# Optimization experiments

Measured on AMD Instinct MI355X. Metric: run time of the kernel, lower is better.

The kernel has to match this reference:

```python
import jax, jax.numpy as jnp
import numpy as np

N, D = 8192, 2        # n_samples, embedding dim (== init dim)
K = 32                # k_base with strategy='fixed' -> static topk size
ALPHA = 1.0           # alpha.item() in forward -> constant
NOISE_SCALE = 0.01
EPS = 1e-8


def setup_inputs() -> dict:
    key = jax.random.key(0)
    x = jax.random.normal(key, (N, D), dtype=jnp.float32)
    return {"x": x}


def _forward(x):
    # torch.std is unbiased (ddof=1)
    mean = jnp.mean(x, axis=0, keepdims=True)          # [1, D]
    std = jnp.std(x, axis=0, keepdims=True, ddof=1)    # [1, D]
    xc = x - mean

    # pairwise Euclidean distances (torch.cdist, p=2): [N, N]
    sq = jnp.sum(xc * xc, axis=1)
    d2 = sq[:, None] + sq[None, :] - 2.0 * (xc @ xc.T)
    dists = jnp.sqrt(jnp.maximum(d2, 0.0))

    # kth-smallest distance per row -> per-point bandwidth sigma
    neg_topk, _ = jax.lax.top_k(-dists, K)             # smallest K (incl. self)
    sigma = -neg_topk[:, -1][:, None]                  # [N, 1]

    # adaptive-bandwidth kernel, row-normalized
    kernel = jnp.exp(-dists / (2.0 * sigma ** 2 + EPS))
    kernel = kernel / (jnp.sum(kernel, axis=1, keepdims=True) + EPS)

    drift = kernel @ xc                                # [N, D]

    step = float(D) ** (-ALPHA)                        # dim ** (-alpha)
    noise = jax.random.normal(jax.random.key(42), xc.shape, dtype=xc.dtype) * NOISE_SCALE
    h = xc + step * (drift - xc) + noise

    # restore original per-feature scale and location
    cur_std = jnp.std(h, axis=0, keepdims=True, ddof=1)
    h = h * (std / (cur_std + EPS))
    return h + mean


def reference(x):
    return _forward(x)
```

## Files before the change

kernel.cpp:

```cpp
#include <hip/hip_runtime.h>
#include <stdint.h>
#include <math.h>

#define N_PTS 8192
#define WPB   16
#define TPB   (WPB * 64)
#define NBLK  (N_PTS / WPB)
#define GRIDC 64
#define NCELL (GRIDC * GRIDC)
#define CW    (9.0f / 64.0f)
#define CINV  (64.0f / 9.0f)

typedef __fp16 h2 __attribute__((ext_vector_type(2)));
typedef uint32_t u32;

__device__ __forceinline__ u32 pksub(u32 a, u32 b) {
  u32 d;
  asm("v_pk_add_f16 %0, %1, %2 neg_lo:[0,1] neg_hi:[0,1]" : "=v"(d) : "v"(a), "v"(b));
  return d;
}
__device__ __forceinline__ float dot2u(u32 a, u32 b, float c) {
#if __has_builtin(__builtin_amdgcn_fdot2)
  return __builtin_amdgcn_fdot2(__builtin_bit_cast(h2, a), __builtin_bit_cast(h2, b), c, false);
#else
  h2 x = __builtin_bit_cast(h2, a), y = __builtin_bit_cast(h2, b);
  return fmaf((float)x.x, (float)y.x, fmaf((float)x.y, (float)y.y, c));
#endif
}
__device__ __forceinline__ u32 cvtpk(float a, float b) {
  return __builtin_bit_cast(u32, __builtin_amdgcn_cvt_pkrtz(a, b));
}
__device__ __forceinline__ int cellc(float v) {
  int c = (int)floorf((v + 4.5f) * CINV);
  return c < 0 ? 0 : (c > GRIDC - 1 ? GRIDC - 1 : c);
}

__device__ __forceinline__ uint32_t rotl32(uint32_t x, int r) {
  return (x << r) | (x >> (32 - r));
}
__device__ __forceinline__ uint32_t threefry_bits(uint32_t idx) {
  const uint32_t k0 = 0u, k1 = 42u;
  const uint32_t k2c = k0 ^ k1 ^ 0x1BD11BDAu;
  uint32_t x0 = 0u, x1 = idx;
  x0 += k0; x1 += k1;
  x0 += x1; x1 = rotl32(x1, 13); x1 ^= x0;
  x0 += x1; x1 = rotl32(x1, 15); x1 ^= x0;
  x0 += x1; x1 = rotl32(x1, 26); x1 ^= x0;
  x0 += x1; x1 = rotl32(x1,  6); x1 ^= x0;
  x0 += k1; x1 += k2c + 1u;
  x0 += x1; x1 = rotl32(x1, 17); x1 ^= x0;
  x0 += x1; x1 = rotl32(x1, 29); x1 ^= x0;
  x0 += x1; x1 = rotl32(x1, 16); x1 ^= x0;
  x0 += x1; x1 = rotl32(x1, 24); x1 ^= x0;
  x0 += k2c; x1 += k0 + 2u;
  x0 += x1; x1 = rotl32(x1, 13); x1 ^= x0;
  x0 += x1; x1 = rotl32(x1, 15); x1 ^= x0;
  x0 += x1; x1 = rotl32(x1, 26); x1 ^= x0;
  x0 += x1; x1 = rotl32(x1,  6); x1 ^= x0;
  x0 += k0; x1 += k1 + 3u;
  x0 += x1; x1 = rotl32(x1, 17); x1 ^= x0;
  x0 += x1; x1 = rotl32(x1, 29); x1 ^= x0;
  x0 += x1; x1 = rotl32(x1, 16); x1 ^= x0;
  x0 += x1; x1 = rotl32(x1, 24); x1 ^= x0;
  x0 += k1; x1 += k2c + 4u;
  x0 += x1; x1 = rotl32(x1, 13); x1 ^= x0;
  x0 += x1; x1 = rotl32(x1, 15); x1 ^= x0;
  x0 += x1; x1 = rotl32(x1, 26); x1 ^= x0;
  x0 += x1; x1 = rotl32(x1,  6); x1 ^= x0;
  x0 += k2c; x1 += k0 + 5u;
  return x0 ^ x1;
}
__device__ __forceinline__ float erfinv_xla(float x) {
  float w = -log1pf(-x * x);
  float p;
  if (w < 5.0f) {
    w -= 2.5f;
    p = 2.81022636e-08f;
    p = fmaf(p, w, 3.43273939e-07f);
    p = fmaf(p, w, -3.5233877e-06f);
    p = fmaf(p, w, -4.39150654e-06f);
    p = fmaf(p, w, 0.00021858087f);
    p = fmaf(p, w, -0.00125372503f);
    p = fmaf(p, w, -0.00417768164f);
    p = fmaf(p, w, 0.246640727f);
    p = fmaf(p, w, 1.50140941f);
  } else {
    w = sqrtf(w) - 3.0f;
    p = -0.000200214257f;
    p = fmaf(p, w, 0.000100950558f);
    p = fmaf(p, w, 0.00134934322f);
    p = fmaf(p, w, -0.00367342844f);
    p = fmaf(p, w, 0.00573950773f);
    p = fmaf(p, w, -0.0076224613f);
    p = fmaf(p, w, 0.00943887047f);
    p = fmaf(p, w, 1.00167406f);
    p = fmaf(p, w, 2.83297682f);
  }
  return p * x;
}
__device__ __forceinline__ float jax_noise(uint32_t idx) {
  uint32_t bits = threefry_bits(idx);
  float uf = __uint_as_float((bits >> 9) | 0x3F800000u) - 1.0f;
  const float lo_u = -0.99999994f;
  float u = fmaxf(lo_u, fmaf(uf, 2.0f, lo_u));
  return 1.4142135623730951f * erfinv_xla(u) * 0.01f;
}

__global__ __launch_bounds__(1024) void build1_kernel(const float* __restrict__ x,
                                                      float* __restrict__ stats,
                                                      u32* __restrict__ base,
                                                      u32* __restrict__ cursor,
                                                      u32* __restrict__ iimg) {
  __shared__ u32 baseL[NCELL];
  __shared__ u32 ssc[1024];
  __shared__ double sred[16][4];
  const int t = threadIdx.x;

#pragma unroll
  for (int k = 0; k < 4; ++k) baseL[t * 4 + k] = 0;
  __syncthreads();

  double s0 = 0, s1 = 0, q0 = 0, q1 = 0;
#pragma unroll
  for (int k = 0; k < 8; ++k) {
    float2 p = ((const float2*)x)[t * 8 + k];
    int cell = cellc(p.y) * GRIDC + cellc(p.x);
    atomicAdd(&baseL[cell], 1u);
    s0 += (double)p.x; s1 += (double)p.y;
    q0 += (double)p.x * (double)p.x; q1 += (double)p.y * (double)p.y;
  }
#pragma unroll
  for (int m = 1; m < 64; m <<= 1) {
    s0 += __shfl_xor(s0, m); s1 += __shfl_xor(s1, m);
    q0 += __shfl_xor(q0, m); q1 += __shfl_xor(q1, m);
  }
  if ((t & 63) == 0) {
    sred[t >> 6][0] = s0; sred[t >> 6][1] = s1;
    sred[t >> 6][2] = q0; sred[t >> 6][3] = q1;
  }
  __syncthreads();

  u32 c0 = baseL[t * 4], c1 = baseL[t * 4 + 1], c2 = baseL[t * 4 + 2], c3 = baseL[t * 4 + 3];
  u32 sum = c0 + c1 + c2 + c3;
  ssc[t] = sum;
  __syncthreads();
  for (int off = 1; off < 1024; off <<= 1) {
    u32 v = (t >= off) ? ssc[t - off] : 0u;
    __syncthreads();
    ssc[t] += v;
    __syncthreads();
  }
  u32 run = ssc[t] - sum;
  u32 b0 = run, b1 = run + c0, b2 = b1 + c1, b3 = b2 + c2;
  __syncthreads();
  baseL[t * 4] = b0; baseL[t * 4 + 1] = b1; baseL[t * 4 + 2] = b2; baseL[t * 4 + 3] = b3;
  base[t * 4] = b0;   base[t * 4 + 1] = b1;   base[t * 4 + 2] = b2;   base[t * 4 + 3] = b3;
  cursor[t * 4] = b0; cursor[t * 4 + 1] = b1; cursor[t * 4 + 2] = b2; cursor[t * 4 + 3] = b3;
  if (t == 1023) base[NCELL] = N_PTS;
  if (t == 0) {
    double a0 = 0, a1 = 0, d0 = 0, d1 = 0;
    for (int k = 0; k < 16; ++k) {
      a0 += sred[k][0]; a1 += sred[k][1]; d0 += sred[k][2]; d1 += sred[k][3];
    }
    double n = (double)N_PTS, m0 = a0 / n, m1 = a1 / n;
    stats[0] = (float)m0; stats[1] = (float)m1;
    stats[2] = (float)sqrt((d0 - n * m0 * m0) / (n - 1.0));
    stats[3] = (float)sqrt((d1 - n * m1 * m1) / (n - 1.0));
  }
  __syncthreads();

  if (t <= 64) {
    u32 acc = 0;
    iimg[t] = 0;
    for (int yy = 0; yy < GRIDC; ++yy) {
      int idx = yy * GRIDC + t;
      u32 v = (idx < NCELL) ? baseL[idx] : (u32)N_PTS;
      acc += v - baseL[yy * GRIDC];
      iimg[(yy + 1) * 65 + t] = acc;
    }
  }
}

__global__ __launch_bounds__(256) void place_kernel(const float* __restrict__ x,
                                                    u32* __restrict__ cursor,
                                                    u32* __restrict__ tmp_pt,
                                                    u32* __restrict__ tmp_ci) {
  int i = blockIdx.x * 256 + threadIdx.x;
  float2 p = ((const float2*)x)[i];
  int cell = cellc(p.y) * GRIDC + cellc(p.x);
  u32 slot = atomicAdd(&cursor[cell], 1u);
  tmp_pt[slot] = cvtpk(p.x, p.y);
  tmp_ci[slot] = ((u32)cell << 13) | (u32)i;
}

__global__ __launch_bounds__(256) void rank_kernel(const u32* __restrict__ base,
                                                   const u32* __restrict__ tmp_pt,
                                                   const u32* __restrict__ tmp_ci,
                                                   u32* __restrict__ spt,
                                                   unsigned short* __restrict__ sidx) {
  int s = blockIdx.x * 256 + threadIdx.x;
  u32 v = tmp_ci[s];
  u32 cell = v >> 13, i = v & 8191u;
  u32 lo = base[cell], hi = base[cell + 1];
  u32 rank = 0;
  for (u32 j = lo; j < hi; ++j) rank += ((tmp_ci[j] & 8191u) < i) ? 1u : 0u;
  u32 d = lo + rank;
  spt[d] = tmp_pt[s];
  sidx[d] = (unsigned short)i;
}

__global__ __launch_bounds__(TPB, 2) void main_kernel(const float* __restrict__ x,
                                                      const float* __restrict__ stats,
                                                      const u32* __restrict__ base,
                                                      const u32* __restrict__ iimg,
                                                      const u32* __restrict__ spt,
                                                      const unsigned short* __restrict__ sidx,
                                                      float* __restrict__ hbuf) {
  __shared__ u32 sptL[N_PTS];
  __shared__ u32 baseL[NCELL + 1];
  __shared__ u32 iimgL[65 * 65];
  const int t = threadIdx.x;
  const int w = t >> 6;
  const int s = t & 63;

#pragma unroll
  for (int k = 0; k < 2; ++k)
    ((uint4*)sptL)[k * TPB + t] = ((const uint4*)spt)[k * TPB + t];
#pragma unroll
  for (int k = 0; k < 4; ++k) baseL[k * TPB + t] = base[k * TPB + t];
  if (t == 0) baseL[NCELL] = N_PTS;
#pragma unroll
  for (int k = 0; k < 5; ++k) {
    int i = k * TPB + t;
    if (i < 65 * 65) iimgL[i] = iimg[i];
  }
  __syncthreads();

  const int p = w * NBLK + blockIdx.x;
  const int orig = (int)sidx[p];
  const float2 xg = ((const float2*)x)[orig];
  const u32 xihu = cvtpk(xg.x, xg.y);
  const int cx = cellc(xg.x), cy = cellc(xg.y);
  const float INF = 3.402823466e+38f;
  const uint4* v4 = (const uint4*)sptL;

  int r = 1;
  bool fullA = false;
  for (;;) {
    int cxl = max(cx - r, 0), cxh = min(cx + r, GRIDC - 1);
    int cyl = max(cy - r, 0), cyh = min(cy + r, GRIDC - 1);
    u32 c = iimgL[(cyh + 1) * 65 + cxh + 1] - iimgL[cyl * 65 + cxh + 1]
          - iimgL[(cyh + 1) * 65 + cxl] + iimgL[cyl * 65 + cxl];
    if (c >= 160u) break;
    int nr = (3 * r + 1) >> 1;
    if (nr > 11) { fullA = true; break; }
    r = nr;
  }

  float d2k;
  for (;;) {
    float r0 = INF, r1 = INF, r2 = INF, r3 = INF, r4 = INF, r5 = INF;
    int cxl, cxh, cyl, cyh;
    if (fullA) { cxl = 0; cxh = GRIDC - 1; cyl = 0; cyh = GRIDC - 1; }
    else {
      cxl = max(cx - r, 0); cxh = min(cx + r, GRIDC - 1);
      cyl = max(cy - r, 0); cyh = min(cy + r, GRIDC - 1);
    }
#define INS6(d2)                      \
    r5 = fminf(fmaxf(r4, d2), r5);    \
    r4 = fminf(fmaxf(r3, d2), r4);    \
    r3 = fminf(fmaxf(r2, d2), r3);    \
    r2 = fminf(fmaxf(r1, d2), r2);    \
    r1 = fminf(fmaxf(r0, d2), r1);    \
    r0 = fminf(r0, d2);
#define DQ(qp, dd) { u32 e = pksub(xihu, qp); dd = dot2u(e, e, 0.0f); }
    if (fullA) {
      for (u32 it = 0; it < 16; ++it) {
        uint4 a = v4[it * 128 + (u32)s];
        uint4 b = v4[it * 128 + 64 + (u32)s];
        float d0, d1, d2, d3, d4, d5, d6, d7;
        DQ(a.x, d0) DQ(a.y, d1) DQ(a.z, d2) DQ(a.w, d3)
        DQ(b.x, d4) DQ(b.y, d5) DQ(b.z, d6) DQ(b.w, d7)
        INS6(d0) INS6(d1) INS6(d2) INS6(d3)
        INS6(d4) INS6(d5) INS6(d6) INS6(d7)
      }
    } else {
      u32 acc = 0;
      for (int yy = cyl; yy <= cyh; ++yy) {
        const int rowb = yy << 6;
        u32 lo = baseL[rowb + cxl];
        u32 len = baseL[rowb + cxh + 1] - lo;
        u32 k = ((u32)s - acc) & 63u;
        for (; k + 192u < len; k += 256u) {
          u32 qa = sptL[lo + k];
          u32 qb = sptL[lo + k + 64u];
          u32 qc = sptL[lo + k + 128u];
          u32 qd = sptL[lo + k + 192u];
          float da, db, dc, dd;
          DQ(qa, da) DQ(qb, db) DQ(qc, dc) DQ(qd, dd)
          INS6(da) INS6(db) INS6(dc) INS6(dd)
        }
        for (; k < len; k += 64u) {
          u32 qa = sptL[lo + k];
          float da;
          DQ(qa, da)
          INS6(da)
        }
        acc += len;
      }
    }
#undef DQ
#undef INS6
    u32 b0 = (u32)__builtin_bit_cast(unsigned short, (__fp16)r0);
    u32 b1 = (u32)__builtin_bit_cast(unsigned short, (__fp16)r1);
    u32 b2 = (u32)__builtin_bit_cast(unsigned short, (__fp16)r2);
    u32 b3 = (u32)__builtin_bit_cast(unsigned short, (__fp16)r3);
    u32 b4 = (u32)__builtin_bit_cast(unsigned short, (__fp16)r4);
    u32 b5 = (u32)__builtin_bit_cast(unsigned short, (__fp16)r5);
    u32 blo = 0u, bhi = 0x7C01u;
    for (int it = 0; it < 15; ++it) {
      u32 mid = (blo + bhi) >> 1;
      int c = __popcll(__ballot(b0 < mid)) + __popcll(__ballot(b1 < mid)) +
              __popcll(__ballot(b2 < mid)) + __popcll(__ballot(b3 < mid)) +
              __popcll(__ballot(b4 < mid)) + __popcll(__ballot(b5 < mid));
      bool ge = (c >= 32);
      bhi = ge ? mid : bhi;
      blo = ge ? blo : mid;
    }
    unsigned short v32 = (unsigned short)(bhi - 1u);
    d2k = (float)__builtin_bit_cast(__fp16, v32);

    float d32 = sqrtf(d2k) + 1e-2f;
    float mxl = (cxl > 0) ? xg.x - (-4.5f + cxl * CW) : 1e9f;
    float mxh = (cxh < GRIDC - 1) ? (-4.5f + (cxh + 1) * CW) - xg.x : 1e9f;
    float myl = (cyl > 0) ? xg.y - (-4.5f + cyl * CW) : 1e9f;
    float myh = (cyh < GRIDC - 1) ? (-4.5f + (cyh + 1) * CW) - xg.y : 1e9f;
    float margin = fminf(fminf(mxl, mxh), fminf(myl, myh));
    if (d32 <= margin) break;
    int nr = (3 * r + 1) >> 1;
    if (nr > 11) fullA = true; else r = nr;
  }

  const float den = fmaf(2.0f, d2k, 1e-8f);
  const float nc1 = -1.4426950408889634f / den;
  const float dcut = 9.704f * den;

  float sw0 = 0.f, swx0 = 0.f, swy0 = 0.f;
  float sw1 = 0.f, swx1 = 0.f, swy1 = 0.f;
  {
    const int bxl = cellc(xg.x - dcut), bxh = cellc(xg.x + dcut);
    const int byl = cellc(xg.y - dcut), byh = cellc(xg.y + dcut);
    const bool fullB = (byh - byl + 1 > 20);
#define WACC0(qp)                                                    \
    {                                                                \
      u32 e = pksub(xihu, qp);                                       \
      float d = __builtin_amdgcn_sqrtf(dot2u(e, e, 0.0f));           \
      float wgt = __builtin_amdgcn_exp2f(fmaf(nc1, d, 10.0f));       \
      h2 ph = __builtin_bit_cast(h2, qp);                            \
      sw0 += wgt;                                                    \
      swx0 = fmaf(wgt, (float)ph.x, swx0);                           \
      swy0 = fmaf(wgt, (float)ph.y, swy0);                           \
    }
#define WACC1(qp)                                                    \
    {                                                                \
      u32 e = pksub(xihu, qp);                                       \
      float d = __builtin_amdgcn_sqrtf(dot2u(e, e, 0.0f));           \
      float wgt = __builtin_amdgcn_exp2f(fmaf(nc1, d, 10.0f));       \
      h2 ph = __builtin_bit_cast(h2, qp);                            \
      sw1 += wgt;                                                    \
      swx1 = fmaf(wgt, (float)ph.x, swx1);                           \
      swy1 = fmaf(wgt, (float)ph.y, swy1);                           \
    }
    if (fullB) {
      for (u32 it = 0; it < 16; ++it) {
        uint4 a = v4[it * 128 + (u32)s];
        uint4 b = v4[it * 128 + 64 + (u32)s];
        WACC0(a.x) WACC1(a.y) WACC0(a.z) WACC1(a.w)
        WACC0(b.x) WACC1(b.y) WACC0(b.z) WACC1(b.w)
      }
    } else {
      u32 acc = 0;
      for (int yy = byl; yy <= byh; ++yy) {
        const int rowb = yy << 6;
        u32 lo = baseL[rowb + bxl];
        u32 len = baseL[rowb + bxh + 1] - lo;
        u32 k = ((u32)s - acc) & 63u;
        for (; k + 64u < len; k += 128u) {
          u32 qa = sptL[lo + k];
          u32 qb = sptL[lo + k + 64u];
          WACC0(qa) WACC1(qb)
        }
        if (k < len) { u32 qa = sptL[lo + k]; WACC0(qa) }
        acc += len;
      }
    }
#undef WACC0
#undef WACC1
  }
  float sw = sw0 + sw1, swx = swx0 + swx1, swy = swy0 + swy1;
#pragma unroll
  for (int m = 1; m < 64; m <<= 1) {
    sw  += __shfl_xor(sw,  m);
    swx += __shfl_xor(swx, m);
    swy += __shfl_xor(swy, m);
  }

  if (s < 2) {
    const float mean = stats[s];
    float inv   = 1.0f / (sw + 1e-8f);
    float drift = (s == 0 ? swx : swy) * inv - mean;
    float xcv   = (s == 0 ? xg.x : xg.y) - mean;
    uint32_t idx = 2u * (uint32_t)orig + (uint32_t)s;
    hbuf[idx] = fmaf(0.5f, drift - xcv, xcv) + jax_noise(idx);
  }
}

__global__ __launch_bounds__(256) void scalefinal_kernel(const float* __restrict__ stats,
                                                         const float* __restrict__ hbuf,
                                                         float* __restrict__ out) {
  __shared__ double red[256][4];
  __shared__ float sc[2];
  const int t = threadIdx.x;
  double s0 = 0, s1 = 0, q0 = 0, q1 = 0;
#pragma unroll
  for (int k = 0; k < 32; ++k) {
    float2 v = ((const float2*)hbuf)[t + k * 256];
    s0 += (double)v.x; s1 += (double)v.y;
    q0 += (double)v.x * (double)v.x; q1 += (double)v.y * (double)v.y;
  }
  red[t][0] = s0; red[t][1] = s1; red[t][2] = q0; red[t][3] = q1;
  __syncthreads();
  for (int st = 128; st > 0; st >>= 1) {
    if (t < st) {
      red[t][0] += red[t + st][0]; red[t][1] += red[t + st][1];
      red[t][2] += red[t + st][2]; red[t][3] += red[t + st][3];
    }
    __syncthreads();
  }
  if (t < 2) {
    double n = (double)N_PTS;
    double m = red[0][t] / n;
    double v = (red[0][2 + t] - n * m * m) / (n - 1.0);
    sc[t] = stats[2 + t] / ((float)sqrt(v) + 1e-8f);
  }
  __syncthreads();
  int i = blockIdx.x * 256 + t;
  int d = i & 1;
  out[i] = fmaf(hbuf[i], sc[d], stats[d]);
}

extern "C" void kernel_launch(void* const* d_in, const int* in_sizes, int n_in,
                              void* d_out, int out_size, void* d_ws, size_t ws_size,
                              hipStream_t stream) {
  const float* x = (const float*)d_in[0];
  float* out = (float*)d_out;
  char* W = (char*)d_ws;
  float* stats = (float*)W;
  u32* base   = (u32*)(W + 128);
  u32* cursor = (u32*)(W + 16640);
  u32* iimg   = (u32*)(W + 33152);
  unsigned short* sidx = (unsigned short*)(W + 50176);
  u32* tmp_pt = (u32*)(W + 66560);
  u32* tmp_ci = (u32*)(W + 99328);
  u32* spt    = (u32*)(W + 132096);
  float* hbuf = (float*)(W + 66560);

  build1_kernel<<<1, 1024, 0, stream>>>(x, stats, base, cursor, iimg);
  place_kernel<<<N_PTS / 256, 256, 0, stream>>>(x, cursor, tmp_pt, tmp_ci);
  rank_kernel<<<N_PTS / 256, 256, 0, stream>>>(base, tmp_pt, tmp_ci, spt, sidx);
  main_kernel<<<NBLK, TPB, 0, stream>>>(x, stats, base, iimg, spt, sidx, hbuf);
  scalefinal_kernel<<<16384 / 256, 256, 0, stream>>>(stats, hbuf, out);
}
```

Before: 52.74 us.

## Fuse grid build, placement and ranking into main kernel with redundant per-block setup

```diff
diff --git a/kernel.cpp b/kernel.cpp
--- a/kernel.cpp
+++ b/kernel.cpp
@@ -4,8 +4,8 @@
 
 #define N_PTS 8192
 #define WPB   16
-#define TPB   (WPB * 64)
-#define NBLK  (N_PTS / WPB)
+#define TPB   1024
+#define NBLK  512
 #define GRIDC 64
 #define NCELL (GRIDC * GRIDC)
 #define CW    (9.0f / 64.0f)
@@ -13,6 +13,7 @@
 
 typedef __fp16 h2 __attribute__((ext_vector_type(2)));
 typedef uint32_t u32;
+typedef unsigned short u16;
 
 __device__ __forceinline__ u32 pksub(u32 a, u32 b) {
   u32 d;
@@ -106,138 +107,124 @@
   return 1.4142135623730951f * erfinv_xla(u) * 0.01f;
 }
 
-__global__ __launch_bounds__(1024) void build1_kernel(const float* __restrict__ x,
+__global__ __launch_bounds__(TPB, 8) void mega_kernel(const float* __restrict__ x,
                                                       float* __restrict__ stats,
-                                                      u32* __restrict__ base,
-                                                      u32* __restrict__ cursor,
-                                                      u32* __restrict__ iimg) {
-  __shared__ u32 baseL[NCELL];
-  __shared__ u32 ssc[1024];
-  __shared__ double sred[16][4];
+                                                      float* __restrict__ hbuf) {
+  __shared__ u32 sptL[N_PTS];
+  __shared__ u32 cursS[NCELL];
+  __shared__ u16 baseS[NCELL + 2];
+  __shared__ u16 tmpS[N_PTS];
+  __shared__ double sredL[16][4];
+  __shared__ float meanS[2];
+
   const int t = threadIdx.x;
-
-#pragma unroll
-  for (int k = 0; k < 4; ++k) baseL[t * 4 + k] = 0;
-  __syncthreads();
-
+  const int w = t >> 6;
+  const int s = t & 63;
+
+#pragma unroll
+  for (int k = 0; k < 4; ++k) cursS[k * TPB + t] = 0;
+
+  u32 pk[8];
+  int cells[8];
   double s0 = 0, s1 = 0, q0 = 0, q1 = 0;
 #pragma unroll
-  for (int k = 0; k < 8; ++k) {
-    float2 p = ((const float2*)x)[t * 8 + k];
-    int cell = cellc(p.y) * GRIDC + cellc(p.x);
-    atomicAdd(&baseL[cell], 1u);
-    s0 += (double)p.x; s1 += (double)p.y;
-    q0 += (double)p.x * (double)p.x; q1 += (double)p.y * (double)p.y;
-  }
+  for (int k = 0; k < 4; ++k) {
+    float4 v = ((const float4*)x)[k * TPB + t];
+    cells[2 * k]     = cellc(v.y) * GRIDC + cellc(v.x);
+    cells[2 * k + 1] = cellc(v.w) * GRIDC + cellc(v.z);
+    pk[2 * k]     = cvtpk(v.x, v.y);
+    pk[2 * k + 1] = cvtpk(v.z, v.w);
+    s0 += (double)v.x + (double)v.z;
+    s1 += (double)v.y + (double)v.w;
+    q0 += fma((double)v.x, (double)v.x, (double)v.z * (double)v.z);
+    q1 += fma((double)v.y, (double)v.y, (double)v.w * (double)v.w);
+  }
+  __syncthreads();
+
+#pragma unroll
+  for (int k = 0; k < 8; ++k) atomicAdd(&cursS[cells[k]], 1u);
+
 #pragma unroll
   for (int m = 1; m < 64; m <<= 1) {
     s0 += __shfl_xor(s0, m); s1 += __shfl_xor(s1, m);
     q0 += __shfl_xor(q0, m); q1 += __shfl_xor(q1, m);
   }
-  if ((t & 63) == 0) {
-    sred[t >> 6][0] = s0; sred[t >> 6][1] = s1;
-    sred[t >> 6][2] = q0; sred[t >> 6][3] = q1;
-  }
-  __syncthreads();
-
-  u32 c0 = baseL[t * 4], c1 = baseL[t * 4 + 1], c2 = baseL[t * 4 + 2], c3 = baseL[t * 4 + 3];
-  u32 sum = c0 + c1 + c2 + c3;
-  ssc[t] = sum;
-  __syncthreads();
-  for (int off = 1; off < 1024; off <<= 1) {
-    u32 v = (t >= off) ? ssc[t - off] : 0u;
+  if (s == 0) { sredL[w][0] = s0; sredL[w][1] = s1; sredL[w][2] = q0; sredL[w][3] = q1; }
+  __syncthreads();
+
+  {
+    u32* ssc = sptL;
+    u32 c0 = cursS[t * 4], c1 = cursS[t * 4 + 1], c2 = cursS[t * 4 + 2], c3 = cursS[t * 4 + 3];
+    u32 sum = c0 + c1 + c2 + c3;
+    ssc[t] = sum;
     __syncthreads();
-    ssc[t] += v;
+    for (int off = 1; off < 1024; off <<= 1) {
+      u32 v = (t >= off) ? ssc[t - off] : 0u;
+      __syncthreads();
+      ssc[t] += v;
+      __syncthreads();
+    }
+    u32 run = ssc[t] - sum;
+    u32 b0 = run, b1 = run + c0, b2 = b1 + c1, b3 = b2 + c2;
     __syncthreads();
-  }
-  u32 run = ssc[t] - sum;
-  u32 b0 = run, b1 = run + c0, b2 = b1 + c1, b3 = b2 + c2;
-  __syncthreads();
-  baseL[t * 4] = b0; baseL[t * 4 + 1] = b1; baseL[t * 4 + 2] = b2; baseL[t * 4 + 3] = b3;
-  base[t * 4] = b0;   base[t * 4 + 1] = b1;   base[t * 4 + 2] = b2;   base[t * 4 + 3] = b3;
-  cursor[t * 4] = b0; cursor[t * 4 + 1] = b1; cursor[t * 4 + 2] = b2; cursor[t * 4 + 3] = b3;
-  if (t == 1023) base[NCELL] = N_PTS;
-  if (t == 0) {
-    double a0 = 0, a1 = 0, d0 = 0, d1 = 0;
-    for (int k = 0; k < 16; ++k) {
-      a0 += sred[k][0]; a1 += sred[k][1]; d0 += sred[k][2]; d1 += sred[k][3];
-    }
-    double n = (double)N_PTS, m0 = a0 / n, m1 = a1 / n;
-    stats[0] = (float)m0; stats[1] = (float)m1;
-    stats[2] = (float)sqrt((d0 - n * m0 * m0) / (n - 1.0));
-    stats[3] = (float)sqrt((d1 - n * m1 * m1) / (n - 1.0));
-  }
-  __syncthreads();
-
+    baseS[t * 4] = (u16)b0; baseS[t * 4 + 1] = (u16)b1;
+    baseS[t * 4 + 2] = (u16)b2; baseS[t * 4 + 3] = (u16)b3;
+    cursS[t * 4] = b0; cursS[t * 4 + 1] = b1; cursS[t * 4 + 2] = b2; cursS[t * 4 + 3] = b3;
+    if (t == 0) {
+      baseS[NCELL] = (u16)N_PTS;
+      double a0 = 0, a1 = 0, d0 = 0, d1 = 0;
+      for (int k = 0; k < 16; ++k) {
+        a0 += sredL[k][0]; a1 += sredL[k][1]; d0 += sredL[k][2]; d1 += sredL[k][3];
+      }
+      double n = (double)N_PTS, m0 = a0 / n, m1 = a1 / n;
+      meanS[0] = (float)m0; meanS[1] = (float)m1;
+      if (blockIdx.x == 0) {
+        stats[0] = (float)m0; stats[1] = (float)m1;
+        stats[2] = (float)sqrt((d0 - n * m0 * m0) / (n - 1.0));
+        stats[3] = (float)sqrt((d1 - n * m1 * m1) / (n - 1.0));
+      }
+    }
+    __syncthreads();
+  }
+
+#pragma unroll
+  for (int k = 0; k < 4; ++k) {
+    u32 sl0 = atomicAdd(&cursS[cells[2 * k]], 1u);
+    tmpS[sl0] = (u16)(2 * (k * TPB + t));
+    u32 sl1 = atomicAdd(&cursS[cells[2 * k + 1]], 1u);
+    tmpS[sl1] = (u16)(2 * (k * TPB + t) + 1);
+  }
+  __syncthreads();
+
+  u16* sidxL = (u16*)cursS;
+#pragma unroll
+  for (int k = 0; k < 8; ++k) {
+    u32 i = (u32)(2 * ((k >> 1) * TPB + t) + (k & 1));
+    int c = cells[k];
+    u32 lo = baseS[c], hi = baseS[c + 1];
+    u32 rk = 0;
+    for (u32 j = lo; j < hi; ++j) rk += ((u32)tmpS[j] < i) ? 1u : 0u;
+    u32 d = lo + rk;
+    sptL[d] = pk[k];
+    sidxL[d] = (u16)i;
+  }
+  __syncthreads();
+
+  u16* iimgS = tmpS;
   if (t <= 64) {
     u32 acc = 0;
-    iimg[t] = 0;
+    iimgS[t] = 0;
     for (int yy = 0; yy < GRIDC; ++yy) {
       int idx = yy * GRIDC + t;
-      u32 v = (idx < NCELL) ? baseL[idx] : (u32)N_PTS;
-      acc += v - baseL[yy * GRIDC];
-      iimg[(yy + 1) * 65 + t] = acc;
-    }
-  }
-}
-
-__global__ __launch_bounds__(256) void place_kernel(const float* __restrict__ x,
-                                                    u32* __restrict__ cursor,
-                                                    u32* __restrict__ tmp_pt,
-                                                    u32* __restrict__ tmp_ci) {
-  int i = blockIdx.x * 256 + threadIdx.x;
-  float2 p = ((const float2*)x)[i];
-  int cell = cellc(p.y) * GRIDC + cellc(p.x);
-  u32 slot = atomicAdd(&cursor[cell], 1u);
-  tmp_pt[slot] = cvtpk(p.x, p.y);
-  tmp_ci[slot] = ((u32)cell << 13) | (u32)i;
-}
-
-__global__ __launch_bounds__(256) void rank_kernel(const u32* __restrict__ base,
-                                                   const u32* __restrict__ tmp_pt,
-                                                   const u32* __restrict__ tmp_ci,
-                                                   u32* __restrict__ spt,
-                                                   unsigned short* __restrict__ sidx) {
-  int s = blockIdx.x * 256 + threadIdx.x;
-  u32 v = tmp_ci[s];
-  u32 cell = v >> 13, i = v & 8191u;
-  u32 lo = base[cell], hi = base[cell + 1];
-  u32 rank = 0;
-  for (u32 j = lo; j < hi; ++j) rank += ((tmp_ci[j] & 8191u) < i) ? 1u : 0u;
-  u32 d = lo + rank;
-  spt[d] = tmp_pt[s];
-  sidx[d] = (unsigned short)i;
-}
-
-__global__ __launch_bounds__(TPB, 2) void main_kernel(const float* __restrict__ x,
-                                                      const float* __restrict__ stats,
-                                                      const u32* __restrict__ base,
-                                                      const u32* __restrict__ iimg,
-                                                      const u32* __restrict__ spt,
-                                                      const unsigned short* __restrict__ sidx,
-                                                      float* __restrict__ hbuf) {
-  __shared__ u32 sptL[N_PTS];
-  __shared__ u32 baseL[NCELL + 1];
-  __shared__ u32 iimgL[65 * 65];
-  const int t = threadIdx.x;
-  const int w = t >> 6;
-  const int s = t & 63;
-
-#pragma unroll
-  for (int k = 0; k < 2; ++k)
-    ((uint4*)sptL)[k * TPB + t] = ((const uint4*)spt)[k * TPB + t];
-#pragma unroll
-  for (int k = 0; k < 4; ++k) baseL[k * TPB + t] = base[k * TPB + t];
-  if (t == 0) baseL[NCELL] = N_PTS;
-#pragma unroll
-  for (int k = 0; k < 5; ++k) {
-    int i = k * TPB + t;
-    if (i < 65 * 65) iimgL[i] = iimg[i];
+      u32 v = (idx < NCELL) ? (u32)baseS[idx] : (u32)N_PTS;
+      acc += v - (u32)baseS[yy * GRIDC];
+      iimgS[(yy + 1) * 65 + t] = (u16)acc;
+    }
   }
   __syncthreads();
 
   const int p = w * NBLK + blockIdx.x;
-  const int orig = (int)sidx[p];
+  const int orig = (int)sidxL[p];
   const float2 xg = ((const float2*)x)[orig];
   const u32 xihu = cvtpk(xg.x, xg.y);
   const int cx = cellc(xg.x), cy = cellc(xg.y);
@@ -249,9 +236,9 @@
   for (;;) {
     int cxl = max(cx - r, 0), cxh = min(cx + r, GRIDC - 1);
     int cyl = max(cy - r, 0), cyh = min(cy + r, GRIDC - 1);
-    u32 c = iimgL[(cyh + 1) * 65 + cxh + 1] - iimgL[cyl * 65 + cxh + 1]
-          - iimgL[(cyh + 1) * 65 + cxl] + iimgL[cyl * 65 + cxl];
-    if (c >= 160u) break;
+    int c = (int)iimgS[(cyh + 1) * 65 + cxh + 1] - (int)iimgS[cyl * 65 + cxh + 1]
+          - (int)iimgS[(cyh + 1) * 65 + cxl] + (int)iimgS[cyl * 65 + cxl];
+    if (c >= 160) break;
     int nr = (3 * r + 1) >> 1;
     if (nr > 11) { fullA = true; break; }
     r = nr;
@@ -288,8 +275,8 @@
       u32 acc = 0;
       for (int yy = cyl; yy <= cyh; ++yy) {
         const int rowb = yy << 6;
-        u32 lo = baseL[rowb + cxl];
-        u32 len = baseL[rowb + cxh + 1] - lo;
+        u32 lo = baseS[rowb + cxl];
+        u32 len = (u32)baseS[rowb + cxh + 1] - lo;
         u32 k = ((u32)s - acc) & 63u;
         for (; k + 192u < len; k += 256u) {
           u32 qa = sptL[lo + k];
@@ -311,12 +298,12 @@
     }
 #undef DQ
 #undef INS6
-    u32 b0 = (u32)__builtin_bit_cast(unsigned short, (__fp16)r0);
-    u32 b1 = (u32)__builtin_bit_cast(unsigned short, (__fp16)r1);
-    u32 b2 = (u32)__builtin_bit_cast(unsigned short, (__fp16)r2);
-    u32 b3 = (u32)__builtin_bit_cast(unsigned short, (__fp16)r3);
-    u32 b4 = (u32)__builtin_bit_cast(unsigned short, (__fp16)r4);
-    u32 b5 = (u32)__builtin_bit_cast(unsigned short, (__fp16)r5);
+    u32 b0 = (u32)__builtin_bit_cast(u16, (__fp16)r0);
+    u32 b1 = (u32)__builtin_bit_cast(u16, (__fp16)r1);
+    u32 b2 = (u32)__builtin_bit_cast(u16, (__fp16)r2);
+    u32 b3 = (u32)__builtin_bit_cast(u16, (__fp16)r3);
+    u32 b4 = (u32)__builtin_bit_cast(u16, (__fp16)r4);
+    u32 b5 = (u32)__builtin_bit_cast(u16, (__fp16)r5);
     u32 blo = 0u, bhi = 0x7C01u;
     for (int it = 0; it < 15; ++it) {
       u32 mid = (blo + bhi) >> 1;
@@ -327,14 +314,21 @@
       bhi = ge ? mid : bhi;
       blo = ge ? blo : mid;
     }
-    unsigned short v32 = (unsigned short)(bhi - 1u);
+    u16 v32 = (u16)(bhi - 1u);
     d2k = (float)__builtin_bit_cast(__fp16, v32);
 
     float d32 = sqrtf(d2k) + 1e-2f;
-    float mxl = (cxl > 0) ? xg.x - (-4.5f + cxl * CW) : 1e9f;
-    float mxh = (cxh < GRIDC - 1) ? (-4.5f + (cxh + 1) * CW) - xg.x : 1e9f;
-    float myl = (cyl > 0) ? xg.y - (-4.5f + cyl * CW) : 1e9f;
-    float myh = (cyh < GRIDC - 1) ? (-4.5f + (cyh + 1) * CW) - xg.y : 1e9f;
+    float mxl = ((fullA ? 0 : max(cx - r, 0)) > 0) ? xg.x - (-4.5f + max(cx - r, 0) * CW) : 1e9f;
+    int cxl2, cxh2, cyl2, cyh2;
+    if (fullA) { cxl2 = 0; cxh2 = GRIDC - 1; cyl2 = 0; cyh2 = GRIDC - 1; }
+    else {
+      cxl2 = max(cx - r, 0); cxh2 = min(cx + r, GRIDC - 1);
+      cyl2 = max(cy - r, 0); cyh2 = min(cy + r, GRIDC - 1);
+    }
+    mxl = (cxl2 > 0) ? xg.x - (-4.5f + cxl2 * CW) : 1e9f;
+    float mxh = (cxh2 < GRIDC - 1) ? (-4.5f + (cxh2 + 1) * CW) - xg.x : 1e9f;
+    float myl = (cyl2 > 0) ? xg.y - (-4.5f + cyl2 * CW) : 1e9f;
+    float myh = (cyh2 < GRIDC - 1) ? (-4.5f + (cyh2 + 1) * CW) - xg.y : 1e9f;
     float margin = fminf(fminf(mxl, mxh), fminf(myl, myh));
     if (d32 <= margin) break;
     int nr = (3 * r + 1) >> 1;
@@ -382,8 +376,8 @@
       u32 acc = 0;
       for (int yy = byl; yy <= byh; ++yy) {
         const int rowb = yy << 6;
-        u32 lo = baseL[rowb + bxl];
-        u32 len = baseL[rowb + bxh + 1] - lo;
+        u32 lo = baseS[rowb + bxl];
+        u32 len = (u32)baseS[rowb + bxh + 1] - lo;
         u32 k = ((u32)s - acc) & 63u;
         for (; k + 64u < len; k += 128u) {
           u32 qa = sptL[lo + k];
@@ -406,7 +400,7 @@
   }
 
   if (s < 2) {
-    const float mean = stats[s];
+    const float mean = meanS[s];
     float inv   = 1.0f / (sw + 1e-8f);
     float drift = (s == 0 ? swx : swy) * inv - mean;
     float xcv   = (s == 0 ? xg.x : xg.y) - mean;
@@ -456,18 +450,8 @@
   float* out = (float*)d_out;
   char* W = (char*)d_ws;
   float* stats = (float*)W;
-  u32* base   = (u32*)(W + 128);
-  u32* cursor = (u32*)(W + 16640);
-  u32* iimg   = (u32*)(W + 33152);
-  unsigned short* sidx = (unsigned short*)(W + 50176);
-  u32* tmp_pt = (u32*)(W + 66560);
-  u32* tmp_ci = (u32*)(W + 99328);
-  u32* spt    = (u32*)(W + 132096);
-  float* hbuf = (float*)(W + 66560);
-
-  build1_kernel<<<1, 1024, 0, stream>>>(x, stats, base, cursor, iimg);
-  place_kernel<<<N_PTS / 256, 256, 0, stream>>>(x, cursor, tmp_pt, tmp_ci);
-  rank_kernel<<<N_PTS / 256, 256, 0, stream>>>(base, tmp_pt, tmp_ci, spt, sidx);
-  main_kernel<<<NBLK, TPB, 0, stream>>>(x, stats, base, iimg, spt, sidx, hbuf);
+  float* hbuf  = (float*)(W + 64);
+
+  mega_kernel<<<NBLK, TPB, 0, stream>>>(x, stats, hbuf);
   scalefinal_kernel<<<16384 / 256, 256, 0, stream>>>(stats, hbuf, out);
 }
```

Result: slower. 79.01 us (+49.8%).
